# Kernel tuning notes

Measured on AMD Instinct MI355X. Metric: run time of the kernel, lower is better.

Reference implementation:

```python
import jax, jax.numpy as jnp
import numpy as np

H = 2048; FF = 8192; NH = 16; HD = 128; R = 16; SCALING = 2.0  # alpha/r = 32/16
EPS = 1e-5
NLEV = 15.0  # 2**4 - 1 levels for 4-bit quantization

def _quantize(key, out_f, in_f):
    # mirrors QuantizedLinear.quantize_weights on a randn*0.02 init weight
    w = jax.random.normal(key, (out_f, in_f), dtype=jnp.float32) * 0.02
    wmin = w.min(axis=1, keepdims=True)
    wmax = w.max(axis=1, keepdims=True)
    rng = jnp.clip(wmax - wmin, 1e-6)
    sc = rng / NLEV
    q = jnp.clip(jnp.round((w - wmin) / sc), 0, NLEV).astype(jnp.int8)
    return q, sc[:, 0], wmin[:, 0]

def setup_inputs():
    key = jax.random.key(0)
    ks = jax.random.split(key, 22)
    dims = [('q', H, H), ('k', H, H), ('v', H, H), ('o', H, H), ('g', FF, H), ('u', FF, H), ('d', H, FF)]
    d = {}
    i = 0
    for name, of, inf in dims:
        qw, sc, zp = _quantize(ks[i], of, inf); i += 1
        d[name + '_qw'] = qw; d[name + '_sc'] = sc; d[name + '_zp'] = zp
        d[name + '_A'] = jax.random.normal(ks[i], (R, inf), dtype=jnp.float32) * 0.01; i += 1
        d[name + '_B'] = jax.random.normal(ks[i], (of, R), dtype=jnp.float32) * 0.01; i += 1
    d['x'] = jax.random.normal(ks[i], (2, 2048, H), dtype=jnp.float32)
    d['ln1_w'] = jnp.ones(H); d['ln1_b'] = jnp.zeros(H)
    d['ln2_w'] = jnp.ones(H); d['ln2_b'] = jnp.zeros(H)
    return d

def _forward(x, qws, ps, lns):
    def lin(h, i):
        sc, zp, A, B = ps[i]
        # dequantize int8 weight (per-row scale/zero-point) + LoRA low-rank update
        W = qws[i].astype(jnp.float32) * sc[:, None] + zp[:, None] + (B @ A) * SCALING
        return h @ W.T
    def ln(h, w, b):
        mu = h.mean(-1, keepdims=True)
        var = h.var(-1, keepdims=True)  # biased, matches torch LayerNorm
        return (h - mu) / jnp.sqrt(var + EPS) * w + b
    ln1_w, ln1_b, ln2_w, ln2_b = lns
    Bsz, S, _ = x.shape
    h = ln(x, ln1_w, ln1_b)
    q = lin(h, 0).reshape(Bsz, S, NH, HD)
    k = lin(h, 1).reshape(Bsz, S, NH, HD)
    v = lin(h, 2).reshape(Bsz, S, NH, HD)
    attn = jnp.einsum('bqhd,bkhd->bhqk', q, k) / (HD ** 0.5)
    attn = jax.nn.softmax(attn, axis=-1)  # dropout is identity in eval
    o = jnp.einsum('bhqk,bkhd->bqhd', attn, v).reshape(Bsz, S, H)
    x1 = x + lin(o, 3)
    h2 = ln(x1, ln2_w, ln2_b)
    ff = jax.nn.silu(lin(h2, 4)) * lin(h2, 5)
    return x1 + lin(ff, 6)

def reference(x, q_qw, q_sc, q_zp, q_A, q_B, k_qw, k_sc, k_zp, k_A, k_B, v_qw, v_sc, v_zp, v_A, v_B, o_qw, o_sc, o_zp, o_A, o_B, g_qw, g_sc, g_zp, g_A, g_B, u_qw, u_sc, u_zp, u_A, u_B, d_qw, d_sc, d_zp, d_A, d_B, ln1_w, ln1_b, ln2_w, ln2_b):
    qws = (q_qw, k_qw, v_qw, o_qw, g_qw, u_qw, d_qw)
    ps = [(q_sc, q_zp, q_A, q_B), (k_sc, k_zp, k_A, k_B), (v_sc, v_zp, v_A, v_B), (o_sc, o_zp, o_A, o_B), (g_sc, g_zp, g_A, g_B), (u_sc, u_zp, u_A, u_B), (d_sc, d_zp, d_A, d_B)]
    return _forward(x, qws, ps, (ln1_w, ln1_b, ln2_w, ln2_b))
```

## Files before the change

kernel.cpp:

```cpp
#include <hip/hip_runtime.h>
#include <cstdint>
#include <cstddef>

#define GLOBAL_AS __attribute__((address_space(1)))
#define LDS_AS    __attribute__((address_space(3)))

typedef __bf16 bf16;
typedef __bf16 bf16x4 __attribute__((ext_vector_type(4)));
typedef __bf16 bf16x8 __attribute__((ext_vector_type(8)));
typedef float  f32x4  __attribute__((ext_vector_type(4)));
typedef int    i32x4  __attribute__((ext_vector_type(4)));
typedef unsigned int u32x2 __attribute__((ext_vector_type(2)));

__device__ __forceinline__ void gl_lds16(const void* g, void* l) {
  __builtin_amdgcn_global_load_lds((GLOBAL_AS void*)g, (LDS_AS void*)l, 16, 0, 0);
}

__global__ __launch_bounds__(256) void ln_kernel(const float* __restrict__ x,
                                                 const float* __restrict__ w,
                                                 const float* __restrict__ bias,
                                                 bf16* __restrict__ out) {
  const int row = blockIdx.x;
  const int tid = threadIdx.x;
  const float* xr = x + (size_t)row * 2048;
  f32x4 v0 = ((const f32x4*)xr)[tid * 2];
  f32x4 v1 = ((const f32x4*)xr)[tid * 2 + 1];
  float s = 0.f, ss = 0.f;
#pragma unroll
  for (int j = 0; j < 4; ++j) { s += v0[j]; ss += v0[j] * v0[j]; }
#pragma unroll
  for (int j = 0; j < 4; ++j) { s += v1[j]; ss += v1[j] * v1[j]; }
#pragma unroll
  for (int d = 1; d < 64; d <<= 1) { s += __shfl_xor(s, d); ss += __shfl_xor(ss, d); }
  __shared__ float red[8];
  const int wave = tid >> 6, lane = tid & 63;
  if (lane == 0) { red[wave * 2] = s; red[wave * 2 + 1] = ss; }
  __syncthreads();
  s  = red[0] + red[2] + red[4] + red[6];
  ss = red[1] + red[3] + red[5] + red[7];
  const float mean = s * (1.f / 2048.f);
  const float var  = ss * (1.f / 2048.f) - mean * mean;
  const float rstd = rsqrtf(var + 1e-5f);
  const int col = tid * 8;
  bf16x8 o;
#pragma unroll
  for (int j = 0; j < 4; ++j) o[j]     = (bf16)((v0[j] - mean) * rstd * w[col + j]     + bias[col + j]);
#pragma unroll
  for (int j = 0; j < 4; ++j) o[4 + j] = (bf16)((v1[j] - mean) * rstd * w[col + 4 + j] + bias[col + 4 + j]);
  *(bf16x8*)(out + (size_t)row * 2048 + col) = o;
}

__global__ __launch_bounds__(256) void ln_q_kernel(const float* __restrict__ x,
    const float* __restrict__ w, const float* __restrict__ bias,
    char* __restrict__ qh, float* __restrict__ s_m, float* __restrict__ rs,
    float* __restrict__ de) {
  const int row = blockIdx.x;
  const int tid = threadIdx.x;
  const float* xr = x + (size_t)row * 2048;
  f32x4 v0 = ((const f32x4*)xr)[tid * 2];
  f32x4 v1 = ((const f32x4*)xr)[tid * 2 + 1];
  float s = 0.f, ss = 0.f;
#pragma unroll
  for (int j = 0; j < 4; ++j) { s += v0[j]; ss += v0[j] * v0[j]; }
#pragma unroll
  for (int j = 0; j < 4; ++j) { s += v1[j]; ss += v1[j] * v1[j]; }
#pragma unroll
  for (int d = 1; d < 64; d <<= 1) { s += __shfl_xor(s, d); ss += __shfl_xor(ss, d); }
  __shared__ float red[12];
  const int wave = tid >> 6, lane = tid & 63;
  if (lane == 0) { red[wave * 2] = s; red[wave * 2 + 1] = ss; }
  __syncthreads();
  s  = red[0] + red[2] + red[4] + red[6];
  ss = red[1] + red[3] + red[5] + red[7];
  const float mean = s * (1.f / 2048.f);
  const float var  = ss * (1.f / 2048.f) - mean * mean;
  const float rstd = rsqrtf(var + 1e-5f);
  const int col = tid * 8;
  float y[8];
#pragma unroll
  for (int j = 0; j < 4; ++j) y[j]     = (v0[j] - mean) * rstd * w[col + j]     + bias[col + j];
#pragma unroll
  for (int j = 0; j < 4; ++j) y[4 + j] = (v1[j] - mean) * rstd * w[col + 4 + j] + bias[col + 4 + j];
  float sy = 0.f, mx = 0.f;
#pragma unroll
  for (int j = 0; j < 8; ++j) { sy += y[j]; mx = fmaxf(mx, fabsf(y[j])); }
#pragma unroll
  for (int d = 1; d < 64; d <<= 1) { sy += __shfl_xor(sy, d); mx = fmaxf(mx, __shfl_xor(mx, d)); }
  __syncthreads();
  if (lane == 0) { red[wave * 2] = sy; red[wave * 2 + 1] = mx; }
  __syncthreads();
  const float sya = red[0] + red[2] + red[4] + red[6];
  const float mxa = fmaxf(fmaxf(red[1], red[3]), fmaxf(red[5], red[7]));
  const float inv = 127.f / fmaxf(mxa, 1e-8f);
  unsigned int lo = 0, hi = 0;
  int qs = 0;
#pragma unroll
  for (int j = 0; j < 4; ++j) { int qi = (int)rintf(y[j] * inv);     qs += qi; lo |= ((unsigned int)qi & 0xffu) << (8 * j); }
#pragma unroll
  for (int j = 0; j < 4; ++j) { int qi = (int)rintf(y[4 + j] * inv); qs += qi; hi |= ((unsigned int)qi & 0xffu) << (8 * j); }
  u32x2 st; st[0] = lo; st[1] = hi;
  *(u32x2*)(qh + (size_t)row * 2048 + col) = st;
  float fqs = (float)qs;
#pragma unroll
  for (int d = 1; d < 64; d <<= 1) fqs += __shfl_xor(fqs, d);
  __syncthreads();
  if (lane == 0) red[8 + wave] = fqs;
  __syncthreads();
  if (tid == 0) {
    const float qsa = red[8] + red[9] + red[10] + red[11];
    const float smv = fmaxf(mxa, 1e-8f) / 127.f;
    s_m[row] = smv; rs[row] = sya; de[row] = sya - smv * qsa;
  }
}

__global__ __launch_bounds__(256) void dequant_kernel(const int* __restrict__ qw,
    const float* __restrict__ sc, const float* __restrict__ zp,
    const float* __restrict__ A, const float* __restrict__ Bm,
    bf16* __restrict__ W, int out_f, int in_f) {
  const int per_row = in_f >> 3;
  const int idx = blockIdx.x * 256 + threadIdx.x;
  const int o  = idx / per_row;
  const int i0 = (idx - o * per_row) << 3;
  const float s = sc[o], z = zp[o];
  float bl[16];
#pragma unroll
  for (int r = 0; r < 16; ++r) bl[r] = Bm[o * 16 + r];
  float acc[8] = {0.f, 0.f, 0.f, 0.f, 0.f, 0.f, 0.f, 0.f};
#pragma unroll
  for (int r = 0; r < 16; ++r) {
    const f32x4* ap = (const f32x4*)(A + (size_t)r * in_f + i0);
    f32x4 a0 = ap[0], a1 = ap[1];
#pragma unroll
    for (int j = 0; j < 4; ++j) { acc[j] += bl[r] * a0[j]; acc[4 + j] += bl[r] * a1[j]; }
  }
  const int* qp = qw + (size_t)o * in_f + i0;
  bf16x8 w8;
#pragma unroll
  for (int j = 0; j < 8; ++j) w8[j] = (bf16)((float)qp[j] * s + z + 2.f * acc[j]);
  *(bf16x8*)(W + (size_t)o * in_f + i0) = w8;
}

__global__ __launch_bounds__(256) void pack_w_kernel(const int* __restrict__ qw,
    const float* __restrict__ sc, char* __restrict__ out, float* __restrict__ wsum) {
  const int row = blockIdx.x;
  const int tid = threadIdx.x;
  const size_t idx = (size_t)row * 2048 + tid * 8;
  i32x4 a = *(const i32x4*)(qw + idx);
  i32x4 b = *(const i32x4*)(qw + idx + 4);
  unsigned int lo = ((unsigned)a[0] & 0xffu) | (((unsigned)a[1] & 0xffu) << 8) |
                    (((unsigned)a[2] & 0xffu) << 16) | (((unsigned)a[3] & 0xffu) << 24);
  unsigned int hi = ((unsigned)b[0] & 0xffu) | (((unsigned)b[1] & 0xffu) << 8) |
                    (((unsigned)b[2] & 0xffu) << 16) | (((unsigned)b[3] & 0xffu) << 24);
  u32x2 st; st[0] = lo; st[1] = hi;
  *(u32x2*)(out + idx) = st;
  float fs = (float)(a[0] + a[1] + a[2] + a[3] + b[0] + b[1] + b[2] + b[3]);
#pragma unroll
  for (int d = 1; d < 64; d <<= 1) fs += __shfl_xor(fs, d);
  __shared__ float red[4];
  const int wave = tid >> 6, lane = tid & 63;
  if (lane == 0) red[wave] = fs;
  __syncthreads();
  if (tid == 0) wsum[row] = sc[row] * (red[0] + red[1] + red[2] + red[3]) * (1.f / 2048.f);
}

__global__ __launch_bounds__(256) void pack_b2_kernel(const float* __restrict__ gB,
    const float* __restrict__ uB, bf16* __restrict__ B2g, bf16* __restrict__ B2u) {
  const int idx = blockIdx.x * 256 + threadIdx.x;
  const int nn = idx >> 5, r = idx & 31;
  B2g[idx] = (r < 16)  ? (bf16)(2.f * gB[nn * 16 + r])        : (bf16)0.f;
  B2u[idx] = (r >= 16) ? (bf16)(2.f * uB[nn * 16 + (r - 16)]) : (bf16)0.f;
}

__global__ __launch_bounds__(256) void hA_kernel(const char* __restrict__ qh,
    const float* __restrict__ s_m, const float* __restrict__ Ag,
    const float* __restrict__ Au, bf16* __restrict__ hA) {
  __shared__ bf16 Asm[32 * 512];
  const int tid = threadIdx.x, wave = tid >> 6, lane = tid & 63;
  const int row = blockIdx.x * 4 + wave;
  float acc[32];
#pragma unroll
  for (int r = 0; r < 32; ++r) acc[r] = 0.f;
  for (int kb = 0; kb < 2048; kb += 512) {
    const int r2 = tid >> 3, c0 = (tid & 7) * 64;
    const float* src = (r2 < 16 ? Ag + (size_t)r2 * 2048 : Au + (size_t)(r2 - 16) * 2048) + kb + c0;
#pragma unroll
    for (int j = 0; j < 64; j += 8) {
      f32x4 va = *(const f32x4*)(src + j);
      f32x4 vb = *(const f32x4*)(src + j + 4);
      bf16x8 bv;
#pragma unroll
      for (int jj = 0; jj < 4; ++jj) { bv[jj] = (bf16)va[jj]; bv[4 + jj] = (bf16)vb[jj]; }
      *(bf16x8*)(Asm + r2 * 512 + c0 + j) = bv;
    }
    __syncthreads();
    float q[8];
    const char* qp = qh + (size_t)row * 2048 + kb + lane * 8;
#pragma unroll
    for (int j = 0; j < 8; ++j) q[j] = (float)qp[j];
#pragma unroll
    for (int r = 0; r < 32; ++r) {
      bf16x8 a8 = *(const bf16x8*)(Asm + r * 512 + lane * 8);
      float d = 0.f;
#pragma unroll
      for (int j = 0; j < 8; ++j) d += q[j] * (float)a8[j];
      acc[r] += d;
    }
    __syncthreads();
  }
  const float s = s_m[row];
#pragma unroll
  for (int r = 0; r < 32; ++r) {
    float v = acc[r];
#pragma unroll
    for (int d = 1; d < 64; d <<= 1) v += __shfl_xor(v, d);
    if (lane == 0) hA[(size_t)row * 32 + r] = (bf16)(s * v);
  }
}

template <int MODE>
__global__ __launch_bounds__(256) void gemm_kernel(const bf16* __restrict__ A,
    const bf16* __restrict__ B, bf16* __restrict__ Cb, float* __restrict__ Cf,
    const float* __restrict__ res, const bf16* __restrict__ gate, bf16* __restrict__ vt,
    int M, int N, int K, int ldc) {
  const int n0 = blockIdx.x * 128;
  const int m0 = blockIdx.y * 128;
  const int tid = threadIdx.x;
  const int wave = tid >> 6, lane = tid & 63;
  const int lcol = lane & 15, lrow = lane >> 4;
  const int wm = (wave >> 1) * 64, wn = (wave & 1) * 64;
  __shared__ bf16 As[128 * 64];
  __shared__ bf16 Bs[128 * 64];
  f32x4 acc[4][4] = {};
  const int sw = (((lane & 7) ^ ((lane >> 3) & 7))) * 8;
  const bf16* Ag = A + (size_t)(m0 + wave * 32 + (lane >> 3)) * K + sw;
  const bf16* Bg = B + (size_t)(n0 + wave * 32 + (lane >> 3)) * K + sw;
  for (int kt = 0; kt < K; kt += 64) {
#pragma unroll
    for (int r8 = 0; r8 < 4; ++r8) {
      gl_lds16(Ag + (size_t)r8 * 8 * K + kt, As + (wave * 32 + r8 * 8) * 64);
      gl_lds16(Bg + (size_t)r8 * 8 * K + kt, Bs + (wave * 32 + r8 * 8) * 64);
    }
    __syncthreads();
#pragma unroll
    for (int ks = 0; ks < 2; ++ks) {
      bf16x8 af[4], bfr[4];
#pragma unroll
      for (int i = 0; i < 4; ++i)
        af[i]  = *(const bf16x8*)(As + (wm + i * 16 + lcol) * 64 + ((ks * 4 + lrow) ^ (lcol & 7)) * 8);
#pragma unroll
      for (int j = 0; j < 4; ++j)
        bfr[j] = *(const bf16x8*)(Bs + (wn + j * 16 + lcol) * 64 + ((ks * 4 + lrow) ^ (lcol & 7)) * 8);
#pragma unroll
      for (int i = 0; i < 4; ++i)
#pragma unroll
        for (int j = 0; j < 4; ++j)
          acc[i][j] = __builtin_amdgcn_mfma_f32_16x16x32_bf16(af[i], bfr[j], acc[i][j], 0, 0, 0);
    }
    __syncthreads();
  }
#pragma unroll
  for (int i = 0; i < 4; ++i)
#pragma unroll
    for (int j = 0; j < 4; ++j) {
      const int row0 = m0 + wm + i * 16 + lrow * 4;
      const int col  = n0 + wn + j * 16 + lcol;
      if (MODE == 3 && col >= 4096) {
        const int c2 = col - 4096;
        bf16x4 v4;
#pragma unroll
        for (int r = 0; r < 4; ++r) v4[r] = (bf16)acc[i][j][r];
        *(bf16x4*)(vt + (size_t)(((row0 >> 11) * 16 + (c2 >> 7)) * 128 + (c2 & 127)) * 2048
                      + (row0 & 2047)) = v4;
      } else {
#pragma unroll
        for (int r = 0; r < 4; ++r) {
          const int row = row0 + r;
          const float v = acc[i][j][r];
          const size_t idx = (size_t)row * ldc + col;
          if (MODE == 0)      Cb[idx] = (bf16)v;
          else if (MODE == 1) Cf[idx] = res[idx] + v;
          else if (MODE == 2) {
            const float g = (float)gate[idx];
            Cb[idx] = (bf16)((g / (1.f + __expf(-g))) * v);
          } else Cb[idx] = (bf16)v;
        }
      }
    }
}

template <int MODE>
__global__ __launch_bounds__(256) void gemm_i8_kernel(const char* __restrict__ Aq,
    const char* __restrict__ Bq, const float* __restrict__ s_m, const float* __restrict__ rs,
    const float* __restrict__ de, const float* __restrict__ sc, const float* __restrict__ zp,
    const float* __restrict__ wsum, const bf16* __restrict__ hA, const bf16* __restrict__ B2,
    bf16* __restrict__ Cb, const bf16* __restrict__ gate, int M, int N, int K) {
  const int n0 = blockIdx.x * 128;
  const int m0 = blockIdx.y * 128;
  const int tid = threadIdx.x;
  const int wave = tid >> 6, lane = tid & 63;
  const int lcol = lane & 15, lrow = lane >> 4;
  const int wm = (wave >> 1) * 64, wn = (wave & 1) * 64;
  __shared__ char As[128 * 128];
  __shared__ char Bs[128 * 128];
  i32x4 acc[4][4] = {};
  const int sw = (((lane & 7) ^ ((lane >> 3) & 7))) * 16;
  const char* Ag = Aq + (size_t)(m0 + wave * 32 + (lane >> 3)) * K + sw;
  const char* Bg = Bq + (size_t)(n0 + wave * 32 + (lane >> 3)) * K + sw;
  for (int kt = 0; kt < K; kt += 128) {
#pragma unroll
    for (int r8 = 0; r8 < 4; ++r8) {
      gl_lds16(Ag + (size_t)r8 * 8 * K + kt, As + (wave * 32 + r8 * 8) * 128);
      gl_lds16(Bg + (size_t)r8 * 8 * K + kt, Bs + (wave * 32 + r8 * 8) * 128);
    }
    __syncthreads();
#pragma unroll
    for (int ks = 0; ks < 2; ++ks) {
      i32x4 af[4], bfr[4];
#pragma unroll
      for (int i = 0; i < 4; ++i)
        af[i]  = *(const i32x4*)(As + (wm + i * 16 + lcol) * 128 + (((ks * 4 + lrow) ^ (lcol & 7))) * 16);
#pragma unroll
      for (int j = 0; j < 4; ++j)
        bfr[j] = *(const i32x4*)(Bs + (wn + j * 16 + lcol) * 128 + (((ks * 4 + lrow) ^ (lcol & 7))) * 16);
#pragma unroll
      for (int i = 0; i < 4; ++i)
#pragma unroll
        for (int j = 0; j < 4; ++j)
          acc[i][j] = __builtin_amdgcn_mfma_i32_16x16x64_i8(af[i], bfr[j], acc[i][j], 0, 0, 0);
    }
    __syncthreads();
  }
  bf16x8 ha[4], bb[4];
#pragma unroll
  for (int i = 0; i < 4; ++i) ha[i] = *(const bf16x8*)(hA + (size_t)(m0 + wm + i * 16 + lcol) * 32 + lrow * 8);
#pragma unroll
  for (int j = 0; j < 4; ++j) bb[j] = *(const bf16x8*)(B2 + (size_t)(n0 + wn + j * 16 + lcol) * 32 + lrow * 8);
  float scv[4], zpv[4], wsv[4];
#pragma unroll
  for (int j = 0; j < 4; ++j) {
    const int col = n0 + wn + j * 16 + lcol;
    scv[j] = sc[col]; zpv[j] = zp[col]; wsv[j] = wsum[col];
  }
  float smv[4][4], rsv[4][4], dev[4][4];
#pragma unroll
  for (int i = 0; i < 4; ++i)
#pragma unroll
    for (int r = 0; r < 4; ++r) {
      const int row = m0 + wm + i * 16 + lrow * 4 + r;
      smv[i][r] = s_m[row]; rsv[i][r] = rs[row]; dev[i][r] = de[row];
    }
  const f32x4 zero = {0.f, 0.f, 0.f, 0.f};
#pragma unroll
  for (int i = 0; i < 4; ++i)
#pragma unroll
    for (int j = 0; j < 4; ++j) {
      f32x4 L = __builtin_amdgcn_mfma_f32_16x16x32_bf16(ha[i], bb[j], zero, 0, 0, 0);
#pragma unroll
      for (int r = 0; r < 4; ++r) {
        const int row = m0 + wm + i * 16 + lrow * 4 + r;
        const int col = n0 + wn + j * 16 + lcol;
        const float v = scv[j] * smv[i][r] * (float)acc[i][j][r] + zpv[j] * rsv[i][r]
                      + wsv[j] * dev[i][r] + L[r];
        const size_t idx = (size_t)row * N + col;
        if (MODE == 0) Cb[idx] = (bf16)v;
        else {
          const float g = (float)gate[idx];
          Cb[idx] = (bf16)((g / (1.f + __expf(-g))) * v);
        }
      }
    }
}

__global__ __launch_bounds__(256) void attn_kernel(const bf16* __restrict__ Cqk,
                                                   const bf16* __restrict__ VtG,
                                                   bf16* __restrict__ obuf) {
  const int qt = blockIdx.x, h = blockIdx.y, b = blockIdx.z;
  const int tid = threadIdx.x, wave = tid >> 6, lane = tid & 63;
  const int lcol = lane & 15, lrow = lane >> 4;
  const int base_m = b * 2048 + qt * 128;
  __shared__ bf16 Ks[64 * 128];
  __shared__ bf16 Vt[128 * 64];
  __shared__ bf16 Ps[4][32 * 72];
  bf16* ps = Ps[wave];
  bf16x8 qf[2][4];
#pragma unroll
  for (int i = 0; i < 2; ++i)
#pragma unroll
    for (int dk = 0; dk < 4; ++dk)
      qf[i][dk] = *(const bf16x8*)(Cqk + (size_t)(base_m + wave * 32 + i * 16 + lcol) * 4096
                                   + h * 128 + dk * 32 + lrow * 8);
  f32x4 of[2][8] = {};
  float m_run[2][4], l_run[2][4];
#pragma unroll
  for (int i = 0; i < 2; ++i)
#pragma unroll
    for (int r = 0; r < 4; ++r) { m_run[i][r] = -1e30f; l_run[i][r] = 0.f; }
  const float SCL2 = 0.12751874972f;
  const int vswz = (lane & 7) ^ (lane >> 3);

  for (int kt = 0; kt < 2048; kt += 64) {
#pragma unroll
    for (int r4 = 0; r4 < 4; ++r4) {
      const int s_low = r4 * 4 + lrow;
      gl_lds16(Cqk + (size_t)(b * 2048 + kt + wave * 16 + s_low) * 4096 + 2048 + h * 128
                   + (lcol ^ s_low) * 8,
               Ks + (wave * 16 + r4 * 4) * 128);
    }
#pragma unroll
    for (int r8 = 0; r8 < 4; ++r8)
      gl_lds16(VtG + (size_t)((b * 16 + h) * 128 + wave * 32 + r8 * 8 + (lane >> 3)) * 2048
                   + kt + vswz * 8,
               Vt + (wave * 32 + r8 * 8) * 64);
    __syncthreads();

    f32x4 sacc[2][4] = {};
#pragma unroll
    for (int jb = 0; jb < 4; ++jb) {
      bf16x8 kf[4];
#pragma unroll
      for (int dk = 0; dk < 4; ++dk)
        kf[dk] = *(const bf16x8*)(Ks + (jb * 16 + lcol) * 128 + ((dk * 4 + lrow) ^ lcol) * 8);
#pragma unroll
      for (int i = 0; i < 2; ++i)
#pragma unroll
        for (int dk = 0; dk < 4; ++dk)
          sacc[i][jb] = __builtin_amdgcn_mfma_f32_16x16x32_bf16(qf[i][dk], kf[dk], sacc[i][jb], 0, 0, 0);
    }

#pragma unroll
    for (int i = 0; i < 2; ++i) {
      float z[4][4], mx[4];
#pragma unroll
      for (int jb = 0; jb < 4; ++jb)
#pragma unroll
        for (int r = 0; r < 4; ++r) z[jb][r] = sacc[i][jb][r] * SCL2;
#pragma unroll
      for (int r = 0; r < 4; ++r)
        mx[r] = fmaxf(fmaxf(z[0][r], z[1][r]), fmaxf(z[2][r], z[3][r]));
#pragma unroll
      for (int d = 1; d < 16; d <<= 1)
#pragma unroll
        for (int r = 0; r < 4; ++r) mx[r] = fmaxf(mx[r], __shfl_xor(mx[r], d));
#pragma unroll
      for (int r = 0; r < 4; ++r) {
        const float mn = fmaxf(m_run[i][r], mx[r]);
        const float alpha = __builtin_amdgcn_exp2f(m_run[i][r] - mn);
        m_run[i][r] = mn;
        float srow = 0.f;
#pragma unroll
        for (int jb = 0; jb < 4; ++jb) {
          const float p = __builtin_amdgcn_exp2f(z[jb][r] - mn);
          z[jb][r] = p; srow += p;
        }
        l_run[i][r] = l_run[i][r] * alpha + srow;
#pragma unroll
        for (int db = 0; db < 8; ++db) of[i][db][r] *= alpha;
      }
#pragma unroll
      for (int jb = 0; jb < 4; ++jb)
#pragma unroll
        for (int r = 0; r < 4; ++r)
          ps[(i * 16 + lrow * 4 + r) * 72 + jb * 16 + lcol] = (bf16)z[jb][r];
    }

#pragma unroll
    for (int ss = 0; ss < 2; ++ss) {
      bf16x8 a0 = *(const bf16x8*)(ps + (0 * 16 + lcol) * 72 + ss * 32 + lrow * 8);
      bf16x8 a1 = *(const bf16x8*)(ps + (1 * 16 + lcol) * 72 + ss * 32 + lrow * 8);
#pragma unroll
      for (int db = 0; db < 8; ++db) {
        bf16x8 vf = *(const bf16x8*)(Vt + (db * 16 + lcol) * 64 + ((ss * 4 + lrow) ^ (lcol & 7)) * 8);
        of[0][db] = __builtin_amdgcn_mfma_f32_16x16x32_bf16(a0, vf, of[0][db], 0, 0, 0);
        of[1][db] = __builtin_amdgcn_mfma_f32_16x16x32_bf16(a1, vf, of[1][db], 0, 0, 0);
      }
    }
    __syncthreads();
  }
#pragma unroll
  for (int i = 0; i < 2; ++i)
#pragma unroll
    for (int r = 0; r < 4; ++r) {
      float l = l_run[i][r];
#pragma unroll
      for (int d = 1; d < 16; d <<= 1) l += __shfl_xor(l, d);
      const float inv = 1.f / l;
      const size_t rb = (size_t)(base_m + wave * 32 + i * 16 + lrow * 4 + r) * 2048 + h * 128;
#pragma unroll
      for (int db = 0; db < 8; ++db)
        obuf[rb + db * 16 + lcol] = (bf16)(of[i][db][r] * inv);
    }
}

extern "C" void kernel_launch(void* const* d_in, const int* in_sizes, int n_in,
                              void* d_out, int out_size, void* d_ws, size_t ws_size,
                              hipStream_t stream) {
  (void)in_sizes; (void)n_in; (void)out_size; (void)ws_size;
  const int*   q_qw = (const int*)d_in[0];   const float* q_sc = (const float*)d_in[1];
  const float* q_zp = (const float*)d_in[2]; const float* q_A  = (const float*)d_in[3];
  const float* q_B  = (const float*)d_in[4];
  const int*   k_qw = (const int*)d_in[5];   const float* k_sc = (const float*)d_in[6];
  const float* k_zp = (const float*)d_in[7]; const float* k_A  = (const float*)d_in[8];
  const float* k_B  = (const float*)d_in[9];
  const int*   v_qw = (const int*)d_in[10];  const float* v_sc = (const float*)d_in[11];
  const float* v_zp = (const float*)d_in[12];const float* v_A  = (const float*)d_in[13];
  const float* v_B  = (const float*)d_in[14];
  const int*   o_qw = (const int*)d_in[15];  const float* o_sc = (const float*)d_in[16];
  const float* o_zp = (const float*)d_in[17];const float* o_A  = (const float*)d_in[18];
  const float* o_B  = (const float*)d_in[19];
  const int*   g_qw = (const int*)d_in[20];  const float* g_sc = (const float*)d_in[21];
  const float* g_zp = (const float*)d_in[22];const float* g_A  = (const float*)d_in[23];
  const float* g_B  = (const float*)d_in[24];
  const int*   u_qw = (const int*)d_in[25];  const float* u_sc = (const float*)d_in[26];
  const float* u_zp = (const float*)d_in[27];const float* u_A  = (const float*)d_in[28];
  const float* u_B  = (const float*)d_in[29];
  const int*   d_qw = (const int*)d_in[30];  const float* d_sc = (const float*)d_in[31];
  const float* d_zp = (const float*)d_in[32];const float* d_A  = (const float*)d_in[33];
  const float* d_B  = (const float*)d_in[34];
  const float* x    = (const float*)d_in[35];
  const float* ln1w = (const float*)d_in[36];const float* ln1b = (const float*)d_in[37];
  const float* ln2w = (const float*)d_in[38];const float* ln2b = (const float*)d_in[39];

  char* ws = (char*)d_ws;
  bf16* W = (bf16*)ws;
  char* Wg8 = ws;
  char* Wu8 = ws + (size_t)8192 * 2048;
  char* p2  = ws + (size_t)32 * 1024 * 1024;
  bf16* h   = (bf16*)p2;
  char*  qh  = p2;
  float* s_m = (float*)(p2 + 8 * 1024 * 1024);
  float* rs  = (float*)(p2 + 8 * 1024 * 1024 + 16384);
  float* de  = (float*)(p2 + 8 * 1024 * 1024 + 32768);
  bf16*  hA  = (bf16*)(p2 + 8 * 1024 * 1024 + 49152);
  bf16*  B2g = (bf16*)(p2 + 8 * 1024 * 1024 + 49152 + 262144);
  bf16*  B2u = B2g + (size_t)8192 * 32;
  float* wsg = (float*)((char*)(B2u + (size_t)8192 * 32));
  float* wsu = wsg + 8192;
  bf16* C = (bf16*)(ws + (size_t)48 * 1024 * 1024);
  bf16* Cqk = C;
  bf16* VtG = C + (size_t)4096 * 4096;
  bf16* obuf = VtG + (size_t)2 * 16 * 128 * 2048;
  float* x1  = (float*)d_out;
  float* out = (float*)d_out;

  ln_kernel<<<4096, 256, 0, stream>>>(x, ln1w, ln1b, h);
  dequant_kernel<<<2048, 256, 0, stream>>>(q_qw, q_sc, q_zp, q_A, q_B, W, 2048, 2048);
  dequant_kernel<<<2048, 256, 0, stream>>>(k_qw, k_sc, k_zp, k_A, k_B, W + (size_t)2048 * 2048, 2048, 2048);
  dequant_kernel<<<2048, 256, 0, stream>>>(v_qw, v_sc, v_zp, v_A, v_B, W + (size_t)4096 * 2048, 2048, 2048);
  gemm_kernel<3><<<dim3(48, 32), 256, 0, stream>>>(h, W, Cqk, nullptr, nullptr, nullptr, VtG, 4096, 6144, 2048, 4096);
  attn_kernel<<<dim3(16, 16, 2), 256, 0, stream>>>(Cqk, VtG, obuf);
  dequant_kernel<<<2048, 256, 0, stream>>>(o_qw, o_sc, o_zp, o_A, o_B, W, 2048, 2048);
  gemm_kernel<1><<<dim3(16, 32), 256, 0, stream>>>(obuf, W, nullptr, x1, x, nullptr, nullptr, 4096, 2048, 2048, 2048);
  ln_q_kernel<<<4096, 256, 0, stream>>>(x1, ln2w, ln2b, qh, s_m, rs, de);
  hA_kernel<<<1024, 256, 0, stream>>>(qh, s_m, g_A, u_A, hA);
  pack_w_kernel<<<8192, 256, 0, stream>>>(g_qw, g_sc, Wg8, wsg);
  pack_w_kernel<<<8192, 256, 0, stream>>>(u_qw, u_sc, Wu8, wsu);
  pack_b2_kernel<<<1024, 256, 0, stream>>>(g_B, u_B, B2g, B2u);
  gemm_i8_kernel<0><<<dim3(64, 32), 256, 0, stream>>>(qh, Wg8, s_m, rs, de, g_sc, g_zp, wsg, hA, B2g, C, nullptr, 4096, 8192, 2048);
  gemm_i8_kernel<1><<<dim3(64, 32), 256, 0, stream>>>(qh, Wu8, s_m, rs, de, u_sc, u_zp, wsu, hA, B2u, C, C, 4096, 8192, 2048);
  dequant_kernel<<<8192, 256, 0, stream>>>(d_qw, d_sc, d_zp, d_A, d_B, W, 2048, 8192);
  gemm_kernel<1><<<dim3(16, 32), 256, 0, stream>>>(C, W, nullptr, out, x1, nullptr, nullptr, 4096, 2048, 8192, 2048);
}
```

Measured before the change: 1.184 ms.

## Rewrite bf16 GEMM as 8-wave 256x128 triple-buffered pipeline with XCD block swizzle

Replaces the 256-thread 128x128 bf16 GEMM with a 512-thread, 256x128 tile kernel. It triple-buffers LDS, prefetching two K-tiles ahead, and interleaves chunks of the global-to-LDS loads with MFMA phases, using s_setprio and explicit barriers. It also remaps block IDs so consecutive workgroups land on the same XCD region for better L2 reuse, and applies the same remap to the int8 GEMM. The goal is to hide load latency and raise MFMA utilisation. The cost is more LDS use (about 144KB per block) and fragile hand-placed vmcnt waits.

```diff
diff --git a/kernel.cpp b/kernel.cpp
--- a/kernel.cpp
+++ b/kernel.cpp
@@ -217,47 +217,119 @@
   }
 }
 
+#define STAGE_A(t, buf, r8) gl_lds16(Ag + (size_t)(r8) * 8 * K + (size_t)(t) * 64, \
+                                     &As[buf][((wave * 32) + (r8) * 8) * 64])
+#define STAGE_B(t, buf, r8) gl_lds16(Bg + (size_t)(r8) * 8 * K + (size_t)(t) * 64, \
+                                     &Bs[buf][((wave * 16) + (r8) * 8) * 64])
+
 template <int MODE>
-__global__ __launch_bounds__(256) void gemm_kernel(const bf16* __restrict__ A,
+__global__ __launch_bounds__(512, 2) void gemm8_kernel(const bf16* __restrict__ A,
     const bf16* __restrict__ B, bf16* __restrict__ Cb, float* __restrict__ Cf,
-    const float* __restrict__ res, const bf16* __restrict__ gate, bf16* __restrict__ vt,
+    const float* __restrict__ res, bf16* __restrict__ vt,
     int M, int N, int K, int ldc) {
-  const int n0 = blockIdx.x * 128;
-  const int m0 = blockIdx.y * 128;
   const int tid = threadIdx.x;
   const int wave = tid >> 6, lane = tid & 63;
   const int lcol = lane & 15, lrow = lane >> 4;
   const int wm = (wave >> 1) * 64, wn = (wave & 1) * 64;
-  __shared__ bf16 As[128 * 64];
-  __shared__ bf16 Bs[128 * 64];
+  const int nwg = gridDim.x * gridDim.y;
+  const int bid = blockIdx.y * gridDim.x + blockIdx.x;
+  const int swb = (bid & 7) * (nwg >> 3) + (bid >> 3);
+  const int n0 = (swb % gridDim.x) * 128;
+  const int m0 = (swb / gridDim.x) * 256;
+  __shared__ bf16 As[3][256 * 64];
+  __shared__ bf16 Bs[3][128 * 64];
   f32x4 acc[4][4] = {};
-  const int sw = (((lane & 7) ^ ((lane >> 3) & 7))) * 8;
+  const int sw = ((lane & 7) ^ ((lane >> 3) & 7)) * 8;
   const bf16* Ag = A + (size_t)(m0 + wave * 32 + (lane >> 3)) * K + sw;
-  const bf16* Bg = B + (size_t)(n0 + wave * 32 + (lane >> 3)) * K + sw;
-  for (int kt = 0; kt < K; kt += 64) {
-#pragma unroll
-    for (int r8 = 0; r8 < 4; ++r8) {
-      gl_lds16(Ag + (size_t)r8 * 8 * K + kt, As + (wave * 32 + r8 * 8) * 64);
-      gl_lds16(Bg + (size_t)r8 * 8 * K + kt, Bs + (wave * 32 + r8 * 8) * 64);
-    }
-    __syncthreads();
-#pragma unroll
-    for (int ks = 0; ks < 2; ++ks) {
-      bf16x8 af[4], bfr[4];
-#pragma unroll
-      for (int i = 0; i < 4; ++i)
-        af[i]  = *(const bf16x8*)(As + (wm + i * 16 + lcol) * 64 + ((ks * 4 + lrow) ^ (lcol & 7)) * 8);
+  const bf16* Bg = B + (size_t)(n0 + wave * 16 + (lane >> 3)) * K + sw;
+  const int nt = K >> 6;
+
+#pragma unroll
+  for (int r8 = 0; r8 < 4; ++r8) STAGE_A(0, 0, r8);
+  STAGE_B(0, 0, 0); STAGE_B(0, 0, 1);
+#pragma unroll
+  for (int r8 = 0; r8 < 4; ++r8) STAGE_A(1, 1, r8);
+  STAGE_B(1, 1, 0); STAGE_B(1, 1, 1);
+  asm volatile("s_waitcnt vmcnt(6)" ::: "memory");
+  __builtin_amdgcn_s_barrier();
+
+  int cur = 0;
+  for (int t = 0; t < nt; ++t) {
+    const bf16* Ac = As[cur];
+    const bf16* Bc = Bs[cur];
+    const int nx = (cur >= 1) ? cur - 1 : cur + 2;
+    const bool pf = (t + 2 < nt);
+
+    bf16x8 b0[4], a0[2];
+#pragma unroll
+    for (int j = 0; j < 4; ++j)
+      b0[j] = *(const bf16x8*)(Bc + (wn + j * 16 + lcol) * 64 + (lrow ^ (lcol & 7)) * 8);
+#pragma unroll
+    for (int i = 0; i < 2; ++i)
+      a0[i] = *(const bf16x8*)(Ac + (wm + i * 16 + lcol) * 64 + (lrow ^ (lcol & 7)) * 8);
+    if (pf) { STAGE_A(t + 2, nx, 0); STAGE_A(t + 2, nx, 1); }
+    __builtin_amdgcn_s_barrier();
+    __builtin_amdgcn_s_setprio(1);
+#pragma unroll
+    for (int i = 0; i < 2; ++i)
 #pragma unroll
       for (int j = 0; j < 4; ++j)
-        bfr[j] = *(const bf16x8*)(Bs + (wn + j * 16 + lcol) * 64 + ((ks * 4 + lrow) ^ (lcol & 7)) * 8);
-#pragma unroll
-      for (int i = 0; i < 4; ++i)
-#pragma unroll
-        for (int j = 0; j < 4; ++j)
-          acc[i][j] = __builtin_amdgcn_mfma_f32_16x16x32_bf16(af[i], bfr[j], acc[i][j], 0, 0, 0);
-    }
-    __syncthreads();
-  }
+        acc[i][j] = __builtin_amdgcn_mfma_f32_16x16x32_bf16(a0[i], b0[j], acc[i][j], 0, 0, 0);
+    __builtin_amdgcn_s_setprio(0);
+    __builtin_amdgcn_s_barrier();
+
+    bf16x8 a1[2];
+#pragma unroll
+    for (int i = 0; i < 2; ++i)
+      a1[i] = *(const bf16x8*)(Ac + (wm + (i + 2) * 16 + lcol) * 64 + (lrow ^ (lcol & 7)) * 8);
+    if (pf) { STAGE_A(t + 2, nx, 2); STAGE_A(t + 2, nx, 3); }
+    __builtin_amdgcn_s_barrier();
+    __builtin_amdgcn_s_setprio(1);
+#pragma unroll
+    for (int i = 0; i < 2; ++i)
+#pragma unroll
+      for (int j = 0; j < 4; ++j)
+        acc[i + 2][j] = __builtin_amdgcn_mfma_f32_16x16x32_bf16(a1[i], b0[j], acc[i + 2][j], 0, 0, 0);
+    __builtin_amdgcn_s_setprio(0);
+    __builtin_amdgcn_s_barrier();
+
+    bf16x8 b1[4], a2[2];
+#pragma unroll
+    for (int j = 0; j < 4; ++j)
+      b1[j] = *(const bf16x8*)(Bc + (wn + j * 16 + lcol) * 64 + ((4 + lrow) ^ (lcol & 7)) * 8);
+#pragma unroll
+    for (int i = 0; i < 2; ++i)
+      a2[i] = *(const bf16x8*)(Ac + (wm + i * 16 + lcol) * 64 + ((4 + lrow) ^ (lcol & 7)) * 8);
+    if (pf) STAGE_B(t + 2, nx, 0);
+    __builtin_amdgcn_s_barrier();
+    __builtin_amdgcn_s_setprio(1);
+#pragma unroll
+    for (int i = 0; i < 2; ++i)
+#pragma unroll
+      for (int j = 0; j < 4; ++j)
+        acc[i][j] = __builtin_amdgcn_mfma_f32_16x16x32_bf16(a2[i], b1[j], acc[i][j], 0, 0, 0);
+    __builtin_amdgcn_s_setprio(0);
+    __builtin_amdgcn_s_barrier();
+
+    bf16x8 a3[2];
+#pragma unroll
+    for (int i = 0; i < 2; ++i)
+      a3[i] = *(const bf16x8*)(Ac + (wm + (i + 2) * 16 + lcol) * 64 + ((4 + lrow) ^ (lcol & 7)) * 8);
+    if (pf) STAGE_B(t + 2, nx, 1);
+    __builtin_amdgcn_s_barrier();
+    __builtin_amdgcn_s_setprio(1);
+#pragma unroll
+    for (int i = 0; i < 2; ++i)
+#pragma unroll
+      for (int j = 0; j < 4; ++j)
+        acc[i + 2][j] = __builtin_amdgcn_mfma_f32_16x16x32_bf16(a3[i], b1[j], acc[i + 2][j], 0, 0, 0);
+    __builtin_amdgcn_s_setprio(0);
+    if (pf) asm volatile("s_waitcnt vmcnt(6)" ::: "memory");
+    else    asm volatile("s_waitcnt vmcnt(0)" ::: "memory");
+    __builtin_amdgcn_s_barrier();
+    cur = (cur == 2) ? 0 : cur + 1;
+  }
+
 #pragma unroll
   for (int i = 0; i < 4; ++i)
 #pragma unroll
@@ -277,16 +349,14 @@
           const int row = row0 + r;
           const float v = acc[i][j][r];
           const size_t idx = (size_t)row * ldc + col;
-          if (MODE == 0)      Cb[idx] = (bf16)v;
-          else if (MODE == 1) Cf[idx] = res[idx] + v;
-          else if (MODE == 2) {
-            const float g = (float)gate[idx];
-            Cb[idx] = (bf16)((g / (1.f + __expf(-g))) * v);
-          } else Cb[idx] = (bf16)v;
+          if (MODE == 1) Cf[idx] = res[idx] + v;
+          else           Cb[idx] = (bf16)v;
         }
       }
     }
 }
+#undef STAGE_A
+#undef STAGE_B
 
 template <int MODE>
 __global__ __launch_bounds__(256) void gemm_i8_kernel(const char* __restrict__ Aq,
@@ -294,8 +364,11 @@
     const float* __restrict__ de, const float* __restrict__ sc, const float* __restrict__ zp,
     const float* __restrict__ wsum, const bf16* __restrict__ hA, const bf16* __restrict__ B2,
     bf16* __restrict__ Cb, const bf16* __restrict__ gate, int M, int N, int K) {
-  const int n0 = blockIdx.x * 128;
-  const int m0 = blockIdx.y * 128;
+  const int nwg = gridDim.x * gridDim.y;
+  const int bid = blockIdx.y * gridDim.x + blockIdx.x;
+  const int swb = (bid & 7) * (nwg >> 3) + (bid >> 3);
+  const int n0 = (swb % gridDim.x) * 128;
+  const int m0 = (swb / gridDim.x) * 128;
   const int tid = threadIdx.x;
   const int wave = tid >> 6, lane = tid & 63;
   const int lcol = lane & 15, lrow = lane >> 4;
@@ -546,10 +619,10 @@
   dequant_kernel<<<2048, 256, 0, stream>>>(q_qw, q_sc, q_zp, q_A, q_B, W, 2048, 2048);
   dequant_kernel<<<2048, 256, 0, stream>>>(k_qw, k_sc, k_zp, k_A, k_B, W + (size_t)2048 * 2048, 2048, 2048);
   dequant_kernel<<<2048, 256, 0, stream>>>(v_qw, v_sc, v_zp, v_A, v_B, W + (size_t)4096 * 2048, 2048, 2048);
-  gemm_kernel<3><<<dim3(48, 32), 256, 0, stream>>>(h, W, Cqk, nullptr, nullptr, nullptr, VtG, 4096, 6144, 2048, 4096);
+  gemm8_kernel<3><<<dim3(48, 16), 512, 0, stream>>>(h, W, Cqk, nullptr, nullptr, VtG, 4096, 6144, 2048, 4096);
   attn_kernel<<<dim3(16, 16, 2), 256, 0, stream>>>(Cqk, VtG, obuf);
   dequant_kernel<<<2048, 256, 0, stream>>>(o_qw, o_sc, o_zp, o_A, o_B, W, 2048, 2048);
-  gemm_kernel<1><<<dim3(16, 32), 256, 0, stream>>>(obuf, W, nullptr, x1, x, nullptr, nullptr, 4096, 2048, 2048, 2048);
+  gemm8_kernel<1><<<dim3(16, 16), 512, 0, stream>>>(obuf, W, nullptr, x1, x, nullptr, 4096, 2048, 2048, 2048);
   ln_q_kernel<<<4096, 256, 0, stream>>>(x1, ln2w, ln2b, qh, s_m, rs, de);
   hA_kernel<<<1024, 256, 0, stream>>>(qh, s_m, g_A, u_A, hA);
   pack_w_kernel<<<8192, 256, 0, stream>>>(g_qw, g_sc, Wg8, wsg);
@@ -558,5 +631,5 @@
   gemm_i8_kernel<0><<<dim3(64, 32), 256, 0, stream>>>(qh, Wg8, s_m, rs, de, g_sc, g_zp, wsg, hA, B2g, C, nullptr, 4096, 8192, 2048);
   gemm_i8_kernel<1><<<dim3(64, 32), 256, 0, stream>>>(qh, Wu8, s_m, rs, de, u_sc, u_zp, wsu, hA, B2u, C, C, 4096, 8192, 2048);
   dequant_kernel<<<8192, 256, 0, stream>>>(d_qw, d_sc, d_zp, d_A, d_B, W, 2048, 8192);
-  gemm_kernel<1><<<dim3(16, 32), 256, 0, stream>>>(C, W, nullptr, out, x1, nullptr, nullptr, 4096, 2048, 8192, 2048);
-}
+  gemm8_kernel<1><<<dim3(16, 16), 512, 0, stream>>>(C, W, nullptr, out, x1, nullptr, 4096, 2048, 8192, 2048);
+}
```

Measured after the change: 1.241 ms. 4.8% more time.
